# Kernel optimization log

Measured on AMD Instinct MI355X. Metric: run time of the kernel, lower is better.

The kernel has to match this reference:

```python
import jax, jax.numpy as jnp
import numpy as np

B, C, Fd, T = 128, 3, 128, 1000
FM, TM, NF, NT = 12, 15, 2, 2   # freq_mask, time_mask, n_freq, n_time
NOISE_STD = 0.04


def setup_inputs() -> dict:
    key = jax.random.key(0)
    ks = jax.random.split(key, 6)
    x = jax.random.normal(ks[0], (B, C, Fd, T), dtype=jnp.float32)
    noise = jax.random.normal(ks[1], (B, C, Fd, T), dtype=jnp.float32)
    # mask lengths: torch.randint(1, max(2, min(fm, F)))
    f_len = jax.random.randint(ks[2], (B, NF), 1, max(2, min(FM, Fd)), dtype=jnp.int32)
    t_len = jax.random.randint(ks[3], (B, NT), 1, max(2, min(TM, T)), dtype=jnp.int32)
    # mask starts: torch.randint(0, max(1, F - f)) — data-dependent upper bound,
    # realized via uniform * (F - len)
    f0 = (jax.random.uniform(ks[4], (B, NF)) * (Fd - f_len)).astype(jnp.int32)
    t0 = (jax.random.uniform(ks[5], (B, NT)) * (T - t_len)).astype(jnp.int32)
    return {"x": x, "noise": noise, "f0": f0, "f_len": f_len, "t0": t0, "t_len": t_len}


def reference(x, noise, f0, f_len, t0, t_len):
    # x: [B, C, F, T]; additive gaussian noise then per-sample freq/time zero masks
    x = x + noise * NOISE_STD
    fi = jnp.arange(x.shape[2])[None, None, :]                       # [1,1,F]
    fmask = jnp.any((fi >= f0[:, :, None]) & (fi < (f0 + f_len)[:, :, None]), axis=1)  # [B,F]
    ti = jnp.arange(x.shape[3])[None, None, :]                       # [1,1,T]
    tmask = jnp.any((ti >= t0[:, :, None]) & (ti < (t0 + t_len)[:, :, None]), axis=1)  # [B,T]
    keep = (~fmask)[:, None, :, None] & (~tmask)[:, None, None, :]   # [B,1,F,T]
    return x * keep
```

## Files before the change

kernel.cpp:

```cpp
#include <hip/hip_runtime.h>
#include <hip/hip_bf16.h>


#define B 128
#define C 3
#define Fd 128
#define T 1000
#define NOISE_STD 0.04f

typedef float  f32x4 __attribute__((ext_vector_type(4)));
typedef int    i32x2 __attribute__((ext_vector_type(2)));

constexpr int ROWS       = B * C * Fd;
constexpr int V4_PER_ROW = T / 4;
constexpr int NV4        = ROWS * V4_PER_ROW;

__global__ __launch_bounds__(256) void specaug_kernel(
    const float* __restrict__ x, const float* __restrict__ noise,
    const int* __restrict__ f0, const int* __restrict__ f_len,
    const int* __restrict__ t0, const int* __restrict__ t_len,
    float* __restrict__ out)
{
    const int gid    = blockIdx.x * blockDim.x + threadIdx.x;
    const int stride = gridDim.x * blockDim.x;

    for (int i = gid; i < NV4; i += stride) {
        const unsigned row = (unsigned)i / (unsigned)V4_PER_ROW;
        const int rem = i - (int)row * V4_PER_ROW;
        const int b   = (int)(row / (unsigned)(C * Fd));
        const int f   = (int)(row & (Fd - 1));

        const i32x2 fa = reinterpret_cast<const i32x2*>(f0)[b];
        const i32x2 fl = reinterpret_cast<const i32x2*>(f_len)[b];
        const bool fmask = (f >= fa.x && f < fa.x + fl.x) ||
                           (f >= fa.y && f < fa.y + fl.y);

        f32x4* outp = reinterpret_cast<f32x4*>(out) + i;

        if (fmask) {
            f32x4 z = {0.f, 0.f, 0.f, 0.f};
            __builtin_nontemporal_store(z, outp);
            continue;
        }

        const i32x2 ta = reinterpret_cast<const i32x2*>(t0)[b];
        const i32x2 tl = reinterpret_cast<const i32x2*>(t_len)[b];

        const f32x4 xv = reinterpret_cast<const f32x4*>(x)[i];
        const f32x4 nv = reinterpret_cast<const f32x4*>(noise)[i];

        const int t = rem * 4;
        f32x4 ov;
#pragma unroll
        for (int k = 0; k < 4; ++k) {
            const int tt = t + k;
            const bool tmask = (tt >= ta.x && tt < ta.x + tl.x) ||
                               (tt >= ta.y && tt < ta.y + tl.y);
            ov[k] = tmask ? 0.f : fmaf(nv[k], NOISE_STD, xv[k]);
        }
        __builtin_nontemporal_store(ov, outp);
    }
}

extern "C" void kernel_launch(void* const* d_in, const int* in_sizes, int n_in,
                              void* d_out, int out_size, void* d_ws, size_t ws_size,
                              hipStream_t stream)
{
    const float* x     = (const float*)d_in[0];
    const float* noise = (const float*)d_in[1];
    const int*   f0    = (const int*)d_in[2];
    const int*   f_len = (const int*)d_in[3];
    const int*   t0    = (const int*)d_in[4];
    const int*   t_len = (const int*)d_in[5];
    float* out = (float*)d_out;

    const int nblocks = 2048;
    specaug_kernel<<<nblocks, 256, 0, stream>>>(x, noise, f0, f_len, t0, t_len, out);
}
```

Before: 115.9 us.

## Map each workgroup to four rows with per-row masks and batched loads

Replaces the grid-stride loop with one workgroup per group of four rows, where each thread handles one float4 column across all four rows. Mask parameters and the time mask are computed once per thread instead of per element, and the loads for all four rows are issued before any compute, which adds memory-level parallelism. Stores change from nontemporal to regular stores. Six of the 256 threads per block (threads 250 to 255) sit idle, and the launch grows to many small blocks.

```diff
diff --git a/kernel.cpp b/kernel.cpp
--- a/kernel.cpp
+++ b/kernel.cpp
@@ -11,9 +11,10 @@
 typedef float  f32x4 __attribute__((ext_vector_type(4)));
 typedef int    i32x2 __attribute__((ext_vector_type(2)));
 
-constexpr int ROWS       = B * C * Fd;
-constexpr int V4_PER_ROW = T / 4;
-constexpr int NV4        = ROWS * V4_PER_ROW;
+constexpr int ROWS        = B * C * Fd;
+constexpr int V4_PER_ROW  = T / 4;
+constexpr int ROWS_PER_WG = 4;
+constexpr int NBLOCKS     = ROWS / ROWS_PER_WG;
 
 __global__ __launch_bounds__(256) void specaug_kernel(
     const float* __restrict__ x, const float* __restrict__ noise,
@@ -21,44 +22,58 @@
     const int* __restrict__ t0, const int* __restrict__ t_len,
     float* __restrict__ out)
 {
-    const int gid    = blockIdx.x * blockDim.x + threadIdx.x;
-    const int stride = gridDim.x * blockDim.x;
+    const int tid = threadIdx.x;
+    if (tid >= V4_PER_ROW) return;
 
-    for (int i = gid; i < NV4; i += stride) {
-        const unsigned row = (unsigned)i / (unsigned)V4_PER_ROW;
-        const int rem = i - (int)row * V4_PER_ROW;
-        const int b   = (int)(row / (unsigned)(C * Fd));
-        const int f   = (int)(row & (Fd - 1));
+    const int r0 = blockIdx.x * ROWS_PER_WG;
+    const int b  = r0 / (C * Fd);
+    const int fb = r0 & (Fd - 1);
 
-        const i32x2 fa = reinterpret_cast<const i32x2*>(f0)[b];
-        const i32x2 fl = reinterpret_cast<const i32x2*>(f_len)[b];
-        const bool fmask = (f >= fa.x && f < fa.x + fl.x) ||
-                           (f >= fa.y && f < fa.y + fl.y);
+    const i32x2 fa = reinterpret_cast<const i32x2*>(f0)[b];
+    const i32x2 fl = reinterpret_cast<const i32x2*>(f_len)[b];
+    const i32x2 ta = reinterpret_cast<const i32x2*>(t0)[b];
+    const i32x2 tl = reinterpret_cast<const i32x2*>(t_len)[b];
 
-        f32x4* outp = reinterpret_cast<f32x4*>(out) + i;
+    bool fm[ROWS_PER_WG];
+#pragma unroll
+    for (int j = 0; j < ROWS_PER_WG; ++j) {
+        const int f = fb + j;
+        fm[j] = (f >= fa.x && f < fa.x + fl.x) || (f >= fa.y && f < fa.y + fl.y);
+    }
 
-        if (fmask) {
-            f32x4 z = {0.f, 0.f, 0.f, 0.f};
-            __builtin_nontemporal_store(z, outp);
-            continue;
+    const int t = tid * 4;
+    bool tm[4];
+#pragma unroll
+    for (int k = 0; k < 4; ++k) {
+        const int tt = t + k;
+        tm[k] = (tt >= ta.x && tt < ta.x + tl.x) || (tt >= ta.y && tt < ta.y + tl.y);
+    }
+
+    const long long base = (long long)r0 * V4_PER_ROW + tid;
+    const f32x4* xp = reinterpret_cast<const f32x4*>(x) + base;
+    const f32x4* np = reinterpret_cast<const f32x4*>(noise) + base;
+    f32x4*       op = reinterpret_cast<f32x4*>(out) + base;
+
+    f32x4 xv[ROWS_PER_WG], nv[ROWS_PER_WG];
+#pragma unroll
+    for (int j = 0; j < ROWS_PER_WG; ++j) {
+        if (!fm[j]) {
+            xv[j] = xp[j * V4_PER_ROW];
+            nv[j] = np[j * V4_PER_ROW];
         }
+    }
 
-        const i32x2 ta = reinterpret_cast<const i32x2*>(t0)[b];
-        const i32x2 tl = reinterpret_cast<const i32x2*>(t_len)[b];
-
-        const f32x4 xv = reinterpret_cast<const f32x4*>(x)[i];
-        const f32x4 nv = reinterpret_cast<const f32x4*>(noise)[i];
-
-        const int t = rem * 4;
+#pragma unroll
+    for (int j = 0; j < ROWS_PER_WG; ++j) {
         f32x4 ov;
+        if (fm[j]) {
+            ov = (f32x4){0.f, 0.f, 0.f, 0.f};
+        } else {
 #pragma unroll
-        for (int k = 0; k < 4; ++k) {
-            const int tt = t + k;
-            const bool tmask = (tt >= ta.x && tt < ta.x + tl.x) ||
-                               (tt >= ta.y && tt < ta.y + tl.y);
-            ov[k] = tmask ? 0.f : fmaf(nv[k], NOISE_STD, xv[k]);
+            for (int k = 0; k < 4; ++k)
+                ov[k] = tm[k] ? 0.f : fmaf(nv[j][k], NOISE_STD, xv[j][k]);
         }
-        __builtin_nontemporal_store(ov, outp);
+        op[j * V4_PER_ROW] = ov;
     }
 }
 
@@ -74,6 +89,5 @@
     const int*   t_len = (const int*)d_in[5];
     float* out = (float*)d_out;
 
-    const int nblocks = 2048;
-    specaug_kernel<<<nblocks, 256, 0, stream>>>(x, noise, f0, f_len, t0, t_len, out);
+    specaug_kernel<<<NBLOCKS, 256, 0, stream>>>(x, noise, f0, f_len, t0, t_len, out);
 }
```

After: 108.6 us. 6.3% less time.
